# Performance work log

Measured on AMD Instinct MI355X. Metric: run time of the kernel, lower is better.

## Reference

```python
import jax, jax.numpy as jnp
import numpy as np

B, S, D = 4, 2048, 768
H = 12
HD = D // H  # 64


def setup_inputs() -> dict:
    key = jax.random.key(0)
    ks = jax.random.split(key, 7)
    scale = 1.0 / np.sqrt(D)
    return {
        "hidden_states": jax.random.normal(ks[0], (B, S, D), dtype=jnp.float32),
        "Wq": jax.random.normal(ks[1], (D, D), dtype=jnp.float32) * scale,
        "bq": jnp.zeros((D,), dtype=jnp.float32),
        "Wk": jax.random.normal(ks[2], (D, D), dtype=jnp.float32) * scale,
        "bk": jnp.zeros((D,), dtype=jnp.float32),
        "Wv": jax.random.normal(ks[3], (D, D), dtype=jnp.float32) * scale,
        "bv": jnp.zeros((D,), dtype=jnp.float32),
    }


def _split_heads(x):
    # [B, S, D] -> [B, H, S, HD]
    b, s, _ = x.shape
    return x.reshape(b, s, H, HD).transpose(0, 2, 1, 3)


def reference(hidden_states, Wq, bq, Wk, bk, Wv, bv):
    q = _split_heads(hidden_states @ Wq + bq)
    k = _split_heads(hidden_states @ Wk + bk)
    v = _split_heads(hidden_states @ Wv + bv)
    # [B, H, S, S] attention scores (naive full materialization, as in source)
    scores = jnp.einsum("bhqd,bhkd->bhqk", q, k) / jnp.sqrt(jnp.float32(HD))
    attn = jax.nn.softmax(scores, axis=-1)  # dropout = identity (eval)
    ctx = jnp.einsum("bhqk,bhkd->bhqd", attn, v)
    # [B, H, S, HD] -> [B, S, D]
    return ctx.transpose(0, 2, 1, 3).reshape(hidden_states.shape[0], -1, H * HD)
```

## Files before the change

kernel.cpp:

```cpp
#include <hip/hip_runtime.h>
#include <cmath>

#define B_  4
#define S_  2048
#define D_  768
#define H_  12
#define HD_ 64
#define BH_ 48
#define N3_ 2304
#define M_  8192

typedef _Float16 half8  __attribute__((ext_vector_type(8)));
typedef _Float16 half4v __attribute__((ext_vector_type(4)));
typedef __fp16   fp16x2 __attribute__((ext_vector_type(2)));
typedef __fp16   fp16x4 __attribute__((ext_vector_type(4)));
typedef float    floatx4 __attribute__((ext_vector_type(4)));

typedef const unsigned int __attribute__((address_space(1)))* gas_u32;
typedef unsigned int __attribute__((address_space(3)))* las_u32;

#define LOG2E 1.4426950408889634f
#define NEG_C (-5.0f * 1.4426950408889634f)

__global__ void cvt_f32_f16(const float* __restrict__ src,
                            _Float16* __restrict__ dst, int n) {
  int i = (blockIdx.x * blockDim.x + threadIdx.x) * 4;
  if (i < n) {
    float4 v = *(const float4*)(src + i);
    half4v h = {(_Float16)v.x, (_Float16)v.y, (_Float16)v.z, (_Float16)v.w};
    *(half4v*)(dst + i) = h;
  }
}

__global__ __launch_bounds__(256) void transpose_cvt_w3(
    const float* __restrict__ Wq, const float* __restrict__ Wk,
    const float* __restrict__ Wv, _Float16* __restrict__ Wt3) {
  __shared__ float tile[32][33];
  const int which = blockIdx.z;
  const float* W = (which == 0) ? Wq : (which == 1) ? Wk : Wv;
  _Float16* Wt = Wt3 + (size_t)which * D_ * D_;
  const int k0 = blockIdx.x * 32, n0 = blockIdx.y * 32;
  const int r = threadIdx.x >> 3, c4 = (threadIdx.x & 7) * 4;
  float4 v = *(const float4*)(W + (size_t)(k0 + r) * D_ + n0 + c4);
  tile[r][c4 + 0] = v.x; tile[r][c4 + 1] = v.y;
  tile[r][c4 + 2] = v.z; tile[r][c4 + 3] = v.w;
  __syncthreads();
  half4v h = {(_Float16)tile[c4 + 0][r], (_Float16)tile[c4 + 1][r],
              (_Float16)tile[c4 + 2][r], (_Float16)tile[c4 + 3][r]};
  *(half4v*)(Wt + (size_t)(n0 + r) * D_ + k0 + c4) = h;
}

__global__ __launch_bounds__(256, 3) void gemm_qkv(
    const _Float16* __restrict__ Xh, const _Float16* __restrict__ Wt3,
    const float* __restrict__ bq, const float* __restrict__ bk,
    const float* __restrict__ bv,
    _Float16* __restrict__ qo, _Float16* __restrict__ ko,
    _Float16* __restrict__ vto) {
  __shared__ __align__(16) char gsm[36864];
  _Float16* As = (_Float16*)gsm;
  _Float16* Bs = (_Float16*)(gsm + 16384);
  const int tid = threadIdx.x;
  const int w = tid >> 6, lane = tid & 63;
  const int tx = lane & 15, quad = lane >> 4;
  const int nBase = blockIdx.x * 128;
  const int mBase = blockIdx.y * 128;
  const int wm = (w & 1) * 64, wn = (w >> 1) * 64;

  floatx4 acc[4][4];
  #pragma unroll
  for (int i = 0; i < 4; ++i)
    #pragma unroll
    for (int j = 0; j < 4; ++j) acc[i][j] = (floatx4){0.f, 0.f, 0.f, 0.f};

  const int ldRow = lane >> 3;
  const int ldCol = (lane & 7) * 8;

  for (int k0 = 0; k0 < D_; k0 += 64) {
    __syncthreads();
    #pragma unroll
    for (int io = 0; io < 4; ++io) {
      int row = w * 32 + io * 8;
      const _Float16* ga =
          Xh + (size_t)(mBase + row + ldRow) * D_ + k0 + ldCol;
      __builtin_amdgcn_global_load_lds((gas_u32)(const void*)ga,
                                       (las_u32)(void*)&As[row * 64], 16, 0, 0);
      const _Float16* gb =
          Wt3 + (size_t)(nBase + row + ldRow) * D_ + k0 + ldCol;
      __builtin_amdgcn_global_load_lds((gas_u32)(const void*)gb,
                                       (las_u32)(void*)&Bs[row * 64], 16, 0, 0);
    }
    __syncthreads();

    half8 af0[4], af1[4], bf0[4], bf1[4];
    #pragma unroll
    for (int i = 0; i < 4; ++i) {
      af0[i] = *(const half8*)&As[(wm + 16 * i + tx) * 64 + quad * 8];
      af1[i] = *(const half8*)&As[(wm + 16 * i + tx) * 64 + quad * 8 + 32];
    }
    #pragma unroll
    for (int j = 0; j < 4; ++j) {
      bf0[j] = *(const half8*)&Bs[(wn + 16 * j + tx) * 64 + quad * 8];
      bf1[j] = *(const half8*)&Bs[(wn + 16 * j + tx) * 64 + quad * 8 + 32];
    }
    #pragma unroll
    for (int i = 0; i < 4; ++i)
      #pragma unroll
      for (int j = 0; j < 4; ++j) {
        acc[i][j] = __builtin_amdgcn_mfma_f32_16x16x32_f16(af0[i], bf0[j], acc[i][j], 0, 0, 0);
        acc[i][j] = __builtin_amdgcn_mfma_f32_16x16x32_f16(af1[i], bf1[j], acc[i][j], 0, 0, 0);
      }
  }

  const int region = nBase / 768;
  const int b = mBase >> 11;
  const int sBase = mBase & (S_ - 1);

  if (region < 2) {
    const float scale = (region == 0) ? 0.125f * LOG2E : 1.0f;
    const float* bias = (region == 0) ? bq : bk;
    _Float16* dst = (region == 0) ? qo : ko;
    const int nLoc768 = nBase % 768;
    __syncthreads();
    _Float16 (*Ct)[136] = (_Float16(*)[136])gsm;
    #pragma unroll
    for (int j = 0; j < 4; ++j) {
      int nl = wn + 16 * j + tx;
      float bb = bias[nLoc768 + nl];
      #pragma unroll
      for (int i = 0; i < 4; ++i)
        #pragma unroll
        for (int r = 0; r < 4; ++r)
          Ct[wm + 16 * i + quad * 4 + r][nl] = (_Float16)((acc[i][j][r] + bb) * scale);
    }
    __syncthreads();
    #pragma unroll
    for (int io = 0; io < 8; ++io) {
      int idx = io * 256 + tid;
      int ml = idx >> 4;
      int nc = (idx & 15) * 8;
      int n = nLoc768 + nc, h = n >> 6, d = n & 63;
      half8 hv = *(const half8*)&Ct[ml][nc];
      *(half8*)(dst + ((size_t)(b * H_ + h) * S_ + sBase + ml) * HD_ + d) = hv;
    }
  } else {
    __syncthreads();
    _Float16 (*Ct)[144] = (_Float16(*)[144])gsm;
    const int nV = nBase - 1536;
    #pragma unroll
    for (int j = 0; j < 4; ++j) {
      int nl = wn + 16 * j + tx;
      float bb = bv[nV + nl];
      #pragma unroll
      for (int i = 0; i < 4; ++i)
        #pragma unroll
        for (int r = 0; r < 4; ++r)
          Ct[nl][wm + 16 * i + quad * 4 + r] = (_Float16)(acc[i][j][r] + bb);
    }
    __syncthreads();
    #pragma unroll
    for (int io = 0; io < 8; ++io) {
      int idx = io * 256 + tid;
      int nl = idx >> 4;
      int sc = (idx & 15) * 8;
      int n = nV + nl, h = n >> 6, d = n & 63;
      half8 hv = *(const half8*)&Ct[nl][sc];
      *(half8*)(vto + (((size_t)(b * H_ + h) * HD_) + d) * S_ + sBase + sc) = hv;
    }
  }
}

__global__ __launch_bounds__(512, 4) void attn_mfma(
    const _Float16* __restrict__ qh, const _Float16* __restrict__ kh,
    const _Float16* __restrict__ vth, float* __restrict__ out) {
  __shared__ __align__(16) char smem[36864];
  _Float16 (*Ks2)[64][72]  = (_Float16(*)[64][72])smem;
  _Float16 (*Vts2)[64][72] = (_Float16(*)[64][72])(smem + 18432);
  float (*Of)[68] = (float(*)[68])smem;
  float* lbuf = (float*)(smem + 34816);

  const int tid = threadIdx.x;
  const int bh = blockIdx.y;
  const int qBase = blockIdx.x * 128;
  const int w = tid >> 6, lane = tid & 63;
  const int half = w >> 2, wq = w & 3;
  const int tx = lane & 15, quad = lane >> 4;

  const _Float16* kp = kh + (size_t)bh * S_ * HD_;
  const _Float16* vtp = vth + (size_t)bh * HD_ * S_;

  half8 bq[2][2];
  #pragma unroll
  for (int g = 0; g < 2; ++g) {
    const _Float16* qp =
        qh + ((size_t)bh * S_ + qBase + wq * 32 + g * 16 + tx) * HD_;
    bq[g][0] = *(const half8*)(qp + quad * 8);
    bq[g][1] = *(const half8*)(qp + quad * 8 + 32);
  }

  floatx4 o_acc[2][4];
  #pragma unroll
  for (int g = 0; g < 2; ++g)
    #pragma unroll
    for (int j = 0; j < 4; ++j) o_acc[g][j] = (floatx4){0.f, 0.f, 0.f, 0.f};
  float l_loc[2] = {0.f, 0.f};

  const int th = tid & 255;
  const int kr = th >> 3, kc = (th & 7) * 8;

  const int NT = S_ / 128;
  half8 kst[2], vst[2];
  {
    const int kt0 = half * 64;
    #pragma unroll
    for (int io = 0; io < 2; ++io) {
      int row = kr + io * 32;
      kst[io] = *(const half8*)(kp + (size_t)(kt0 + row) * HD_ + kc);
      vst[io] = *(const half8*)(vtp + (size_t)row * S_ + kt0 + kc);
    }
  }

  for (int it = 0; it < NT; ++it) {
    __syncthreads();
    #pragma unroll
    for (int io = 0; io < 2; ++io) {
      int row = kr + io * 32;
      *(half8*)&Ks2[half][row][kc] = kst[io];
      *(half8*)&Vts2[half][row][kc] = vst[io];
    }
    if (it + 1 < NT) {
      const int kt1 = (it + 1) * 128 + half * 64;
      #pragma unroll
      for (int io = 0; io < 2; ++io) {
        int row = kr + io * 32;
        kst[io] = *(const half8*)(kp + (size_t)(kt1 + row) * HD_ + kc);
        vst[io] = *(const half8*)(vtp + (size_t)row * S_ + kt1 + kc);
      }
    }
    __syncthreads();

    #pragma unroll
    for (int t = 0; t < 4; ++t) {
      half8 ka0 = *(const half8*)&Ks2[half][16 * t + tx][quad * 8];
      half8 ka1 = *(const half8*)&Ks2[half][16 * t + tx][quad * 8 + 32];
      fp16x4 pf[2];
      #pragma unroll
      for (int g = 0; g < 2; ++g) {
        __builtin_amdgcn_s_setprio(1);
        floatx4 st = __builtin_amdgcn_mfma_f32_16x16x32_f16(
            ka0, bq[g][0], (floatx4){NEG_C, NEG_C, NEG_C, NEG_C}, 0, 0, 0);
        st = __builtin_amdgcn_mfma_f32_16x16x32_f16(ka1, bq[g][1], st, 0, 0, 0);
        __builtin_amdgcn_s_setprio(0);
        float p0 = __builtin_amdgcn_exp2f(st[0]);
        float p1 = __builtin_amdgcn_exp2f(st[1]);
        float p2 = __builtin_amdgcn_exp2f(st[2]);
        float p3 = __builtin_amdgcn_exp2f(st[3]);
        l_loc[g] += (p0 + p1) + (p2 + p3);
        fp16x2 lo = __builtin_amdgcn_cvt_pkrtz(p0, p1);
        fp16x2 hi = __builtin_amdgcn_cvt_pkrtz(p2, p3);
        pf[g] = (fp16x4){lo.x, lo.y, hi.x, hi.y};
      }
      __builtin_amdgcn_s_setprio(1);
      #pragma unroll
      for (int j = 0; j < 4; ++j) {
        fp16x4 vb = *(const fp16x4*)&Vts2[half][16 * j + tx][16 * t + quad * 4];
        o_acc[0][j] = __builtin_amdgcn_mfma_f32_16x16x16f16(pf[0], vb, o_acc[0][j], 0, 0, 0);
        o_acc[1][j] = __builtin_amdgcn_mfma_f32_16x16x16f16(pf[1], vb, o_acc[1][j], 0, 0, 0);
      }
      __builtin_amdgcn_s_setprio(0);
    }
  }

  float lg[2];
  #pragma unroll
  for (int g = 0; g < 2; ++g) {
    lg[g] = l_loc[g];
    lg[g] += __shfl_xor(lg[g], 16, 64);
    lg[g] += __shfl_xor(lg[g], 32, 64);
  }

  __syncthreads();
  if (half == 1) {
    #pragma unroll
    for (int g = 0; g < 2; ++g) {
      int rowB = wq * 32 + g * 16;
      #pragma unroll
      for (int j = 0; j < 4; ++j)
        #pragma unroll
        for (int r = 0; r < 4; ++r)
          Of[rowB + quad * 4 + r][16 * j + tx] = o_acc[g][j][r];
      if (quad == 0) lbuf[rowB + tx] = lg[g];
    }
  }
  __syncthreads();
  if (half == 0) {
    const int b = bh / H_;
    const int h = bh % H_;
    #pragma unroll
    for (int g = 0; g < 2; ++g) {
      int rowB = wq * 32 + g * 16;
      float ltot = lg[g] + lbuf[rowB + tx];
      #pragma unroll
      for (int r = 0; r < 4; ++r) {
        int m = quad * 4 + r;
        float inv = 1.f / __shfl(ltot, m, 64);
        int s = qBase + rowB + m;
        #pragma unroll
        for (int j = 0; j < 4; ++j) {
          float o = o_acc[g][j][r] + Of[rowB + m][16 * j + tx];
          out[((size_t)b * S_ + s) * D_ + h * HD_ + 16 * j + tx] = o * inv;
        }
      }
    }
  }
}

extern "C" void kernel_launch(void* const* d_in, const int* in_sizes, int n_in,
                              void* d_out, int out_size, void* d_ws, size_t ws_size,
                              hipStream_t stream) {
  const float* X  = (const float*)d_in[0];
  const float* Wq = (const float*)d_in[1];
  const float* bq = (const float*)d_in[2];
  const float* Wk = (const float*)d_in[3];
  const float* bk = (const float*)d_in[4];
  const float* Wv = (const float*)d_in[5];
  const float* bv = (const float*)d_in[6];
  float* out = (float*)d_out;

  const size_t nX = (size_t)M_ * D_;
  const size_t nW = (size_t)D_ * D_;
  const size_t nQ = (size_t)BH_ * S_ * HD_;

  _Float16* Xh  = (_Float16*)d_ws;
  _Float16* Wt3 = Xh + nX;
  _Float16* qhb = Wt3 + 3 * nW;
  _Float16* khb = qhb + nQ;
  _Float16* vtb = khb + nQ;

  cvt_f32_f16<<<(int)(nX / 4 / 256), 256, 0, stream>>>(X, Xh, (int)nX);

  dim3 gridT(D_ / 32, D_ / 32, 3);
  transpose_cvt_w3<<<gridT, 256, 0, stream>>>(Wq, Wk, Wv, Wt3);

  dim3 gridG(N3_ / 128, M_ / 128);
  gemm_qkv<<<gridG, 256, 0, stream>>>(Xh, Wt3, bq, bk, bv, qhb, khb, vtb);

  dim3 gridA(S_ / 128, BH_);
  attn_mfma<<<gridA, 512, 0, stream>>>(qhb, khb, vtb, out);
}
```

Before: 205.8 us.

## Use 16x16x32 MFMA for PV by permuting key rows and swizzling K smem

```diff
diff --git a/kernel.cpp b/kernel.cpp
--- a/kernel.cpp
+++ b/kernel.cpp
@@ -184,6 +184,8 @@
   const int w = tid >> 6, lane = tid & 63;
   const int half = w >> 2, wq = w & 3;
   const int tx = lane & 15, quad = lane >> 4;
+  const int pr  = 8 * (tx >> 2) + (tx & 3);
+  const int kgx = (quad ^ (tx >> 2)) * 8;
 
   const _Float16* kp = kh + (size_t)bh * S_ * HD_;
   const _Float16* vtp = vth + (size_t)bh * HD_ * S_;
@@ -206,6 +208,7 @@
 
   const int th = tid & 255;
   const int kr = th >> 3, kc = (th & 7) * 8;
+  const int skc = ((th & 7) ^ ((kr >> 3) & 3)) * 8;
 
   const int NT = S_ / 128;
   half8 kst[2], vst[2];
@@ -224,7 +227,7 @@
     #pragma unroll
     for (int io = 0; io < 2; ++io) {
       int row = kr + io * 32;
-      *(half8*)&Ks2[half][row][kc] = kst[io];
+      *(half8*)&Ks2[half][row][skc] = kst[io];
       *(half8*)&Vts2[half][row][kc] = vst[io];
     }
     if (it + 1 < NT) {
@@ -239,32 +242,43 @@
     __syncthreads();
 
     #pragma unroll
-    for (int t = 0; t < 4; ++t) {
-      half8 ka0 = *(const half8*)&Ks2[half][16 * t + tx][quad * 8];
-      half8 ka1 = *(const half8*)&Ks2[half][16 * t + tx][quad * 8 + 32];
-      fp16x4 pf[2];
-      #pragma unroll
-      for (int g = 0; g < 2; ++g) {
-        __builtin_amdgcn_s_setprio(1);
-        floatx4 st = __builtin_amdgcn_mfma_f32_16x16x32_f16(
-            ka0, bq[g][0], (floatx4){NEG_C, NEG_C, NEG_C, NEG_C}, 0, 0, 0);
-        st = __builtin_amdgcn_mfma_f32_16x16x32_f16(ka1, bq[g][1], st, 0, 0, 0);
-        __builtin_amdgcn_s_setprio(0);
-        float p0 = __builtin_amdgcn_exp2f(st[0]);
-        float p1 = __builtin_amdgcn_exp2f(st[1]);
-        float p2 = __builtin_amdgcn_exp2f(st[2]);
-        float p3 = __builtin_amdgcn_exp2f(st[3]);
-        l_loc[g] += (p0 + p1) + (p2 + p3);
-        fp16x2 lo = __builtin_amdgcn_cvt_pkrtz(p0, p1);
-        fp16x2 hi = __builtin_amdgcn_cvt_pkrtz(p2, p3);
-        pf[g] = (fp16x4){lo.x, lo.y, hi.x, hi.y};
-      }
+    for (int T = 0; T < 2; ++T) {
+      fp16x2 plo[2][2], phi[2][2];
+      #pragma unroll
+      for (int u = 0; u < 2; ++u) {
+        const int lrow = pr + 4 * u + 32 * T;
+        half8 ka0 = *(const half8*)&Ks2[half][lrow][kgx];
+        half8 ka1 = *(const half8*)&Ks2[half][lrow][kgx + 32];
+        #pragma unroll
+        for (int g = 0; g < 2; ++g) {
+          __builtin_amdgcn_s_setprio(1);
+          floatx4 st = __builtin_amdgcn_mfma_f32_16x16x32_f16(
+              ka0, bq[g][0], (floatx4){NEG_C, NEG_C, NEG_C, NEG_C}, 0, 0, 0);
+          st = __builtin_amdgcn_mfma_f32_16x16x32_f16(ka1, bq[g][1], st, 0, 0, 0);
+          __builtin_amdgcn_s_setprio(0);
+          float p0 = __builtin_amdgcn_exp2f(st[0]);
+          float p1 = __builtin_amdgcn_exp2f(st[1]);
+          float p2 = __builtin_amdgcn_exp2f(st[2]);
+          float p3 = __builtin_amdgcn_exp2f(st[3]);
+          l_loc[g] += (p0 + p1) + (p2 + p3);
+          plo[g][u] = __builtin_amdgcn_cvt_pkrtz(p0, p1);
+          phi[g][u] = __builtin_amdgcn_cvt_pkrtz(p2, p3);
+        }
+      }
+      half8 pf0 = {(_Float16)plo[0][0].x, (_Float16)plo[0][0].y,
+                   (_Float16)phi[0][0].x, (_Float16)phi[0][0].y,
+                   (_Float16)plo[0][1].x, (_Float16)plo[0][1].y,
+                   (_Float16)phi[0][1].x, (_Float16)phi[0][1].y};
+      half8 pf1 = {(_Float16)plo[1][0].x, (_Float16)plo[1][0].y,
+                   (_Float16)phi[1][0].x, (_Float16)phi[1][0].y,
+                   (_Float16)plo[1][1].x, (_Float16)plo[1][1].y,
+                   (_Float16)phi[1][1].x, (_Float16)phi[1][1].y};
       __builtin_amdgcn_s_setprio(1);
       #pragma unroll
       for (int j = 0; j < 4; ++j) {
-        fp16x4 vb = *(const fp16x4*)&Vts2[half][16 * j + tx][16 * t + quad * 4];
-        o_acc[0][j] = __builtin_amdgcn_mfma_f32_16x16x16f16(pf[0], vb, o_acc[0][j], 0, 0, 0);
-        o_acc[1][j] = __builtin_amdgcn_mfma_f32_16x16x16f16(pf[1], vb, o_acc[1][j], 0, 0, 0);
+        half8 vb = *(const half8*)&Vts2[half][16 * j + tx][32 * T + quad * 8];
+        o_acc[0][j] = __builtin_amdgcn_mfma_f32_16x16x32_f16(pf0, vb, o_acc[0][j], 0, 0, 0);
+        o_acc[1][j] = __builtin_amdgcn_mfma_f32_16x16x32_f16(pf1, vb, o_acc[1][j], 0, 0, 0);
       }
       __builtin_amdgcn_s_setprio(0);
     }
```

Result: faster. 196.9 us (-4.3%).
